# Optimization experiments

Measured on AMD Instinct MI355X. Metric: run time of the kernel, lower is better.

Reference implementation:

```python
import jax, jax.numpy as jnp
import numpy as np

D_K = 64

def setup_inputs() -> dict:
    key = jax.random.key(0)
    ks = jax.random.split(key, 8)
    B, C, H, W = 4, 256, 40, 40
    d_k, d_g, n_rel = 64, 64, 16
    s = lambda fan_in: 1.0 / np.sqrt(fan_in)
    return {
        "x":  jax.random.normal(ks[0], (B, C, H, W), jnp.float32),
        "Wq": jax.random.normal(ks[1], (C, d_k), jnp.float32) * s(C),
        "bq": jnp.zeros((d_k,), jnp.float32),
        "Wk": jax.random.normal(ks[2], (C, d_k), jnp.float32) * s(C),
        "bk": jnp.zeros((d_k,), jnp.float32),
        "Wv": jax.random.normal(ks[3], (C, C), jnp.float32) * s(C),
        "bv": jnp.zeros((C,), jnp.float32),
        "Wg1": jax.random.normal(ks[4], (4, d_g), jnp.float32) * s(4),
        "bg1": jnp.zeros((d_g,), jnp.float32),
        "Wg2": jax.random.normal(ks[5], (d_g, d_g), jnp.float32) * s(d_g),
        "bg2": jnp.zeros((d_g,), jnp.float32),
        "Wgr": jax.random.normal(ks[6], (d_g, n_rel), jnp.float32) * s(d_g),
        "bgr": jnp.zeros((n_rel,), jnp.float32),
    }

def reference(x, Wq, bq, Wk, bk, Wv, bv, Wg1, bg1, Wg2, bg2, Wgr, bgr):
    B, C, H, W = x.shape
    N = H * W
    # [B, N, C] feature tokens
    feats = jnp.transpose(x, (0, 2, 3, 1)).reshape(B, N, C)
    # pseudo-bboxes: (x, y, 1, 1) per pixel
    yy, xx = jnp.meshgrid(jnp.arange(H), jnp.arange(W), indexing="ij")
    bboxes = jnp.stack(
        [xx.astype(jnp.float32), yy.astype(jnp.float32),
         jnp.ones((H, W), jnp.float32), jnp.ones((H, W), jnp.float32)],
        axis=-1).reshape(N, 4)
    # pairwise geometric features [N, N, 4]: diff[m, n] = bboxes[n] - bboxes[m]
    diff = bboxes[None, :, :] - bboxes[:, None, :]
    geo = jnp.log(jnp.abs(diff) + 1e-8)
    # geo embedding MLP -> relation weights
    e = jax.nn.relu(geo @ Wg1 + bg1)            # [N, N, d_g]
    e = jax.nn.relu(e @ Wg2 + bg2)              # [N, N, d_g]
    w_g = jax.nn.relu(e @ Wgr + bgr)            # [N, N, n_rel]
    w_g_mean = w_g.mean(axis=2)                 # [N, N]
    # appearance attention
    q = feats @ Wq + bq                         # [B, N, d_k]
    k = feats @ Wk + bk                         # [B, N, d_k]
    w_a = jax.nn.softmax(jnp.einsum("bnd,bmd->bnm", q, k) / jnp.sqrt(jnp.float32(D_K)), axis=2)
    w_mn = w_a * w_g_mean[None]                 # [B, N, N]
    v = feats @ Wv + bv                         # [B, N, C]
    rel = jnp.einsum("bnm,bmc->bnc", w_mn, v)
    aug = feats + rel
    return jnp.transpose(aug.reshape(B, H, W, C), (0, 3, 1, 2))
```

## Files before the change

kernel.cpp:

```cpp
#include <hip/hip_runtime.h>
#include <hip/hip_bf16.h>
#include <math.h>

#define NTOK 1600
#define CDIM 256
#define DK   64

typedef __attribute__((ext_vector_type(8))) short bf16x8;
typedef __attribute__((ext_vector_type(4))) float f32x4;

__device__ inline unsigned short f2bf(float v) {
    unsigned int u = __float_as_uint(v);
    unsigned int r = (u + 0x7fffu + ((u >> 16) & 1u)) >> 16;
    return (unsigned short)r;
}

__global__ __launch_bounds__(256) void geo_table_kernel(
    const float* __restrict__ Wg1, const float* __restrict__ bg1,
    const float* __restrict__ Wg2, const float* __restrict__ bg2,
    const float* __restrict__ Wgr, const float* __restrict__ bgr,
    float* __restrict__ table)
{
    int idx = blockIdx.x * 256 + threadIdx.x;
    if (idx >= NTOK) return;
    int ady = idx / 40, adx = idx % 40;
    float g0 = logf((float)adx + 1e-8f);
    float g1 = logf((float)ady + 1e-8f);
    float gc = logf(1e-8f);

    float e1[64];
    #pragma unroll
    for (int j = 0; j < 64; ++j) {
        float t = g0 * Wg1[0*64 + j] + g1 * Wg1[1*64 + j]
                + gc * (Wg1[2*64 + j] + Wg1[3*64 + j]) + bg1[j];
        e1[j] = fmaxf(t, 0.f);
    }
    float wg[16];
    #pragma unroll
    for (int r = 0; r < 16; ++r) wg[r] = bgr[r];
    for (int j = 0; j < 64; ++j) {
        float t = bg2[j];
        #pragma unroll
        for (int i = 0; i < 64; ++i) t += e1[i] * Wg2[i*64 + j];
        t = fmaxf(t, 0.f);
        #pragma unroll
        for (int r = 0; r < 16; ++r) wg[r] += t * Wgr[j*16 + r];
    }
    float s = 0.f;
    #pragma unroll
    for (int r = 0; r < 16; ++r) s += fmaxf(wg[r], 0.f);
    table[idx] = s * (1.f / 16.f);
}

__global__ __launch_bounds__(256) void qkv_kernel(
    const float* __restrict__ x,
    const float* __restrict__ Wq, const float* __restrict__ bq,
    const float* __restrict__ Wk, const float* __restrict__ bk,
    const float* __restrict__ Wv, const float* __restrict__ bv,
    unsigned short* __restrict__ Qb, unsigned short* __restrict__ Kb,
    unsigned short* __restrict__ Vt)
{
    const int N = NTOK, C = CDIM;
    int bx = blockIdx.x;
    int jt = blockIdx.y;
    int b  = blockIdx.z;

    const float* Wm; const float* bias;
    int jb, stride;
    if (jt == 0)      { Wm = Wq; bias = bq; jb = 0;         stride = 64;  }
    else if (jt == 1) { Wm = Wk; bias = bk; jb = 0;         stride = 64;  }
    else              { Wm = Wv; bias = bv; jb = (jt-2)*64; stride = 256; }

    __shared__ __align__(16) float xs[64*68];
    __shared__ __align__(16) float wm[64*68];

    int t  = threadIdx.x;
    int tn = t & 15;
    int tj = t >> 4;
    int n0 = bx * 64;

    float acc[4][4] = {};

    for (int kc = 0; kc < 4; ++kc) {
        int k0 = kc * 64;
        #pragma unroll
        for (int p = 0; p < 4; ++p) {
            int idx4 = p*256 + t;
            int row = idx4 >> 4, col4 = (idx4 & 15) * 4;
            *(float4*)&xs[row*68 + col4] =
                *(const float4*)&x[(size_t)(b*C + k0 + row)*N + n0 + col4];
            *(float4*)&wm[row*68 + col4] =
                *(const float4*)&Wm[(size_t)(k0 + row)*stride + jb + col4];
        }
        __syncthreads();
        #pragma unroll
        for (int kk = 0; kk < 64; ++kk) {
            float4 xv = *(const float4*)(xs + kk*68 + tn*4);
            float4 wv = *(const float4*)(wm + kk*68 + tj*4);
            acc[0][0] += xv.x*wv.x; acc[0][1] += xv.x*wv.y; acc[0][2] += xv.x*wv.z; acc[0][3] += xv.x*wv.w;
            acc[1][0] += xv.y*wv.x; acc[1][1] += xv.y*wv.y; acc[1][2] += xv.y*wv.z; acc[1][3] += xv.y*wv.w;
            acc[2][0] += xv.z*wv.x; acc[2][1] += xv.z*wv.y; acc[2][2] += xv.z*wv.z; acc[2][3] += xv.z*wv.w;
            acc[3][0] += xv.w*wv.x; acc[3][1] += xv.w*wv.y; acc[3][2] += xv.w*wv.z; acc[3][3] += xv.w*wv.w;
        }
        __syncthreads();
    }

    if (jt <= 1) {
        unsigned short* outb = (jt == 0 ? Qb : Kb) + (size_t)b*N*DK;
        float scale = (jt == 0) ? 0.125f : 1.0f;
        #pragma unroll
        for (int ii = 0; ii < 4; ++ii) {
            int n = n0 + tn*4 + ii;
            __align__(8) unsigned short u[4];
            #pragma unroll
            for (int jj = 0; jj < 4; ++jj)
                u[jj] = f2bf((acc[ii][jj] + bias[tj*4 + jj]) * scale);
            *(uint2*)&outb[(size_t)n*DK + tj*4] = *(const uint2*)u;
        }
    } else {
        #pragma unroll
        for (int ii = 0; ii < 4; ++ii)
            #pragma unroll
            for (int jj = 0; jj < 4; ++jj)
                xs[(tn*4 + ii)*68 + tj*4 + jj] = acc[ii][jj] + bias[jb + tj*4 + jj];
        __syncthreads();
        int jl = t >> 2, nb = (t & 3) * 16;
        __align__(16) unsigned short u[16];
        #pragma unroll
        for (int i = 0; i < 16; ++i)
            u[i] = f2bf(xs[(nb + i)*68 + jl]);
        unsigned short* vrow = Vt + ((size_t)b*C + jb + jl)*N + n0 + nb;
        ((uint4*)vrow)[0] = ((const uint4*)u)[0];
        ((uint4*)vrow)[1] = ((const uint4*)u)[1];
    }
}

__global__ __launch_bounds__(256) void attn_mfma_kernel(
    const float* __restrict__ x, const float* __restrict__ gtab,
    const unsigned short* __restrict__ Qb, const unsigned short* __restrict__ Kb,
    const unsigned short* __restrict__ Vt, float* __restrict__ out)
{
    const int N = NTOK, C = CDIM;
    int b = blockIdx.y, n0 = blockIdx.x * 16;
    int t = threadIdx.x;
    int w = t >> 6, l = t & 63;
    int l15 = l & 15, l4 = l >> 4;

    __shared__ unsigned short Pl[2][16*72];
    __shared__ float sh_g[NTOK];
    __shared__ float shZ[4][16];
    __shared__ __align__(16) float outs[256*17];

    #pragma unroll
    for (int p = 0; p < 7; ++p) { int i = p*256 + t; if (i < NTOK) sh_g[i] = gtab[i]; }

    const unsigned short* qrow = &Qb[((size_t)b*N + n0 + l15)*DK + l4*8];
    bf16x8 qa0 = *(const bf16x8*)qrow;
    bf16x8 qa1 = *(const bf16x8*)(qrow + 32);

    f32x4 acc[4];
    #pragma unroll
    for (int i = 0; i < 4; ++i) acc[i] = (f32x4){0.f, 0.f, 0.f, 0.f};
    float z[4] = {0.f, 0.f, 0.f, 0.f};

    int yn[4], xn[4];
    #pragma unroll
    for (int r = 0; r < 4; ++r) {
        int n = n0 + l4*4 + r;
        yn[r] = n / 40; xn[r] = n - 40*yn[r];
    }
    int mcol = w*16 + l15;

    __syncthreads();

    for (int cc = 0; cc < 25; ++cc) {
        int m0 = cc * 64;
        const unsigned short* kbase = &Kb[((size_t)b*N + m0 + mcol)*DK + l4*8];
        bf16x8 kb0 = *(const bf16x8*)kbase;
        bf16x8 kb1 = *(const bf16x8*)(kbase + 32);
        f32x4 s4 = (f32x4){0.f, 0.f, 0.f, 0.f};
        s4 = __builtin_amdgcn_mfma_f32_16x16x32_bf16(qa0, kb0, s4, 0, 0, 0);
        s4 = __builtin_amdgcn_mfma_f32_16x16x32_bf16(qa1, kb1, s4, 0, 0, 0);

        int mg = m0 + mcol;
        int ym = mg / 40, xm = mg - 40*ym;
        unsigned short* prow = &Pl[cc & 1][0];
        #pragma unroll
        for (int r = 0; r < 4; ++r) {
            float e = __expf(s4[r]);
            z[r] += e;
            int ady = ym - yn[r]; ady = ady < 0 ? -ady : ady;
            int adx = xm - xn[r]; adx = adx < 0 ? -adx : adx;
            float p = e * sh_g[ady*40 + adx];
            prow[(l4*4 + r)*72 + mcol] = f2bf(p);
        }
        __syncthreads();

        const unsigned short* pb = &Pl[cc & 1][l15*72 + l4*8];
        bf16x8 pa0 = *(const bf16x8*)pb;
        bf16x8 pa1 = *(const bf16x8*)(pb + 32);
        #pragma unroll
        for (int t4 = 0; t4 < 4; ++t4) {
            int c0 = w*64 + t4*16 + l15;
            const unsigned short* vb = &Vt[((size_t)b*C + c0)*N + m0 + l4*8];
            bf16x8 v0 = *(const bf16x8*)vb;
            bf16x8 v1 = *(const bf16x8*)(vb + 32);
            acc[t4] = __builtin_amdgcn_mfma_f32_16x16x32_bf16(pa0, v0, acc[t4], 0, 0, 0);
            acc[t4] = __builtin_amdgcn_mfma_f32_16x16x32_bf16(pa1, v1, acc[t4], 0, 0, 0);
        }
    }

    #pragma unroll
    for (int r = 0; r < 4; ++r) {
        float v = z[r];
        v += __shfl_xor(v, 1); v += __shfl_xor(v, 2);
        v += __shfl_xor(v, 4); v += __shfl_xor(v, 8);
        z[r] = v;
    }
    if (l15 == 0) {
        #pragma unroll
        for (int r = 0; r < 4; ++r) shZ[w][l4*4 + r] = z[r];
    }
    __syncthreads();

    float invz[4];
    #pragma unroll
    for (int r = 0; r < 4; ++r) {
        int row = l4*4 + r;
        float s = shZ[0][row] + shZ[1][row] + shZ[2][row] + shZ[3][row];
        invz[r] = 1.f / s;
    }
    #pragma unroll
    for (int t4 = 0; t4 < 4; ++t4)
        #pragma unroll
        for (int r = 0; r < 4; ++r)
            outs[(w*64 + t4*16 + l15)*17 + l4*4 + r] = acc[t4][r] * invz[r];
    __syncthreads();

    #pragma unroll
    for (int p = 0; p < 16; ++p) {
        int c2 = p*16 + (t >> 4), r2 = t & 15;
        size_t gi = (size_t)b*C*N + (size_t)c2*N + n0 + r2;
        out[gi] = x[gi] + outs[c2*17 + r2];
    }
}

extern "C" void kernel_launch(void* const* d_in, const int* in_sizes, int n_in,
                              void* d_out, int out_size, void* d_ws, size_t ws_size,
                              hipStream_t stream)
{
    const float* x   = (const float*)d_in[0];
    const float* Wq  = (const float*)d_in[1];
    const float* bq  = (const float*)d_in[2];
    const float* Wk  = (const float*)d_in[3];
    const float* bk  = (const float*)d_in[4];
    const float* Wv  = (const float*)d_in[5];
    const float* bv  = (const float*)d_in[6];
    const float* Wg1 = (const float*)d_in[7];
    const float* bg1 = (const float*)d_in[8];
    const float* Wg2 = (const float*)d_in[9];
    const float* bg2 = (const float*)d_in[10];
    const float* Wgr = (const float*)d_in[11];
    const float* bgr = (const float*)d_in[12];

    char* ws = (char*)d_ws;
    float* table          = (float*)ws;
    unsigned short* Qb    = (unsigned short*)(ws + 8192);
    unsigned short* Kb    = (unsigned short*)(ws + 8192 + 819200);
    unsigned short* Vt    = (unsigned short*)(ws + 8192 + 2*819200);

    geo_table_kernel<<<dim3(7), dim3(256), 0, stream>>>(Wg1, bg1, Wg2, bg2, Wgr, bgr, table);
    qkv_kernel<<<dim3(25, 6, 4), dim3(256), 0, stream>>>(x, Wq, bq, Wk, bk, Wv, bv, Qb, Kb, Vt);
    attn_mfma_kernel<<<dim3(100, 4), dim3(256), 0, stream>>>(x, table, Qb, Kb, Vt, (float*)d_out);
}
```

Baseline: 209.8 us.

## Parallelize geo table, use MFMA for QKV, split attention over key chunks per wave

The geometric MLP table kernel now assigns one wave per table entry, so hidden units are computed in parallel across lanes with shared-memory staging and shuffle reductions, instead of one thread per entry with a serial 64x64 loop. The QKV projection converts x and weights to bf16 in shared memory and uses bf16 MFMA instead of scalar fp32 FMAs. The attention kernel gives each wave its own key chunks and all 256 output channels, which removes the per-chunk block barrier, and combines partial results with LDS atomics at the end. This costs more accumulator registers, atomic reduction traffic and extra bf16 rounding in the projections.

After: 204.5 us. 2.5% less time.

```diff
diff --git a/kernel.cpp b/kernel.cpp
--- a/kernel.cpp
+++ b/kernel.cpp
@@ -16,40 +16,41 @@
 }
 
 __global__ __launch_bounds__(256) void geo_table_kernel(
-    const float* __restrict__ Wg1, const float* __restrict__ bg1,
-    const float* __restrict__ Wg2, const float* __restrict__ bg2,
+    const float* __restrict__ W1, const float* __restrict__ b1,
+    const float* __restrict__ W2, const float* __restrict__ b2,
     const float* __restrict__ Wgr, const float* __restrict__ bgr,
     float* __restrict__ table)
 {
-    int idx = blockIdx.x * 256 + threadIdx.x;
-    if (idx >= NTOK) return;
+    __shared__ float e1s[4][64];
+    __shared__ float e2s[4][64];
+    int t = threadIdx.x;
+    int w = t >> 6, j = t & 63;
+    int idx = blockIdx.x * 4 + w;
     int ady = idx / 40, adx = idx % 40;
     float g0 = logf((float)adx + 1e-8f);
     float g1 = logf((float)ady + 1e-8f);
     float gc = logf(1e-8f);
 
-    float e1[64];
-    #pragma unroll
-    for (int j = 0; j < 64; ++j) {
-        float t = g0 * Wg1[0*64 + j] + g1 * Wg1[1*64 + j]
-                + gc * (Wg1[2*64 + j] + Wg1[3*64 + j]) + bg1[j];
-        e1[j] = fmaxf(t, 0.f);
-    }
-    float wg[16];
-    #pragma unroll
-    for (int r = 0; r < 16; ++r) wg[r] = bgr[r];
-    for (int j = 0; j < 64; ++j) {
-        float t = bg2[j];
-        #pragma unroll
-        for (int i = 0; i < 64; ++i) t += e1[i] * Wg2[i*64 + j];
-        t = fmaxf(t, 0.f);
-        #pragma unroll
-        for (int r = 0; r < 16; ++r) wg[r] += t * Wgr[j*16 + r];
-    }
-    float s = 0.f;
-    #pragma unroll
-    for (int r = 0; r < 16; ++r) s += fmaxf(wg[r], 0.f);
-    table[idx] = s * (1.f / 16.f);
+    float e1 = fmaxf(g0*W1[j] + g1*W1[64+j] + gc*(W1[128+j]+W1[192+j]) + b1[j], 0.f);
+    e1s[w][j] = e1;
+    __syncthreads();
+
+    float e2 = b2[j];
+    #pragma unroll 8
+    for (int i = 0; i < 64; ++i) e2 += e1s[w][i] * W2[i*64 + j];
+    e2 = fmaxf(e2, 0.f);
+    e2s[w][j] = e2;
+    __syncthreads();
+
+    int r = j & 15, q = j >> 4;
+    float v = (q == 0) ? bgr[r] : 0.f;
+    #pragma unroll
+    for (int i = 0; i < 16; ++i) v += e2s[w][q*16 + i] * Wgr[(q*16 + i)*16 + r];
+    v += __shfl_xor(v, 16); v += __shfl_xor(v, 32);
+    v = fmaxf(v, 0.f);
+    v += __shfl_xor(v, 1); v += __shfl_xor(v, 2);
+    v += __shfl_xor(v, 4); v += __shfl_xor(v, 8);
+    if (j == 0) table[idx] = v * (1.f / 16.f);
 }
 
 __global__ __launch_bounds__(256) void qkv_kernel(
@@ -60,82 +61,88 @@
     unsigned short* __restrict__ Qb, unsigned short* __restrict__ Kb,
     unsigned short* __restrict__ Vt)
 {
-    const int N = NTOK, C = CDIM;
-    int bx = blockIdx.x;
-    int jt = blockIdx.y;
-    int b  = blockIdx.z;
-
-    const float* Wm; const float* bias;
-    int jb, stride;
+    const int N = NTOK;
+    int bx = blockIdx.x, jt = blockIdx.y, b = blockIdx.z;
+    const float* Wm; const float* bias; int jb, stride;
     if (jt == 0)      { Wm = Wq; bias = bq; jb = 0;         stride = 64;  }
     else if (jt == 1) { Wm = Wk; bias = bk; jb = 0;         stride = 64;  }
     else              { Wm = Wv; bias = bv; jb = (jt-2)*64; stride = 256; }
 
-    __shared__ __align__(16) float xs[64*68];
-    __shared__ __align__(16) float wm[64*68];
-
-    int t  = threadIdx.x;
-    int tn = t & 15;
-    int tj = t >> 4;
+    __shared__ __align__(16) unsigned short As[64*72];
+    __shared__ __align__(16) unsigned short Bs[64*72];
+
+    int t = threadIdx.x;
+    int w = t >> 6, l = t & 63;
+    int l15 = l & 15, l4 = l >> 4;
     int n0 = bx * 64;
 
-    float acc[4][4] = {};
+    f32x4 acc[4];
+    #pragma unroll
+    for (int i = 0; i < 4; ++i) acc[i] = (f32x4){0.f,0.f,0.f,0.f};
 
     for (int kc = 0; kc < 4; ++kc) {
         int k0 = kc * 64;
+        __syncthreads();
         #pragma unroll
         for (int p = 0; p < 4; ++p) {
-            int idx4 = p*256 + t;
-            int row = idx4 >> 4, col4 = (idx4 & 15) * 4;
-            *(float4*)&xs[row*68 + col4] =
-                *(const float4*)&x[(size_t)(b*C + k0 + row)*N + n0 + col4];
-            *(float4*)&wm[row*68 + col4] =
-                *(const float4*)&Wm[(size_t)(k0 + row)*stride + jb + col4];
-        }
-        __syncthreads();
-        #pragma unroll
-        for (int kk = 0; kk < 64; ++kk) {
-            float4 xv = *(const float4*)(xs + kk*68 + tn*4);
-            float4 wv = *(const float4*)(wm + kk*68 + tj*4);
-            acc[0][0] += xv.x*wv.x; acc[0][1] += xv.x*wv.y; acc[0][2] += xv.x*wv.z; acc[0][3] += xv.x*wv.w;
-            acc[1][0] += xv.y*wv.x; acc[1][1] += xv.y*wv.y; acc[1][2] += xv.y*wv.z; acc[1][3] += xv.y*wv.w;
-            acc[2][0] += xv.z*wv.x; acc[2][1] += xv.z*wv.y; acc[2][2] += xv.z*wv.z; acc[2][3] += xv.z*wv.w;
-            acc[3][0] += xv.w*wv.x; acc[3][1] += xv.w*wv.y; acc[3][2] += xv.w*wv.z; acc[3][3] += xv.w*wv.w;
-        }
-        __syncthreads();
+            int k = p*16 + (t >> 4);
+            int n4 = (t & 15) * 4;
+            float4 xv = *(const float4*)&x[((size_t)(b*CDIM) + k0 + k)*N + n0 + n4];
+            As[(n4+0)*72 + k] = f2bf(xv.x); As[(n4+1)*72 + k] = f2bf(xv.y);
+            As[(n4+2)*72 + k] = f2bf(xv.z); As[(n4+3)*72 + k] = f2bf(xv.w);
+            float4 wv = *(const float4*)&Wm[(size_t)(k0 + k)*stride + jb + n4];
+            Bs[(n4+0)*72 + k] = f2bf(wv.x); Bs[(n4+1)*72 + k] = f2bf(wv.y);
+            Bs[(n4+2)*72 + k] = f2bf(wv.z); Bs[(n4+3)*72 + k] = f2bf(wv.w);
+        }
+        __syncthreads();
+        #pragma unroll
+        for (int ks = 0; ks < 2; ++ks) {
+            bf16x8 a = *(const bf16x8*)&As[(w*16 + l15)*72 + ks*32 + l4*8];
+            #pragma unroll
+            for (int jt4 = 0; jt4 < 4; ++jt4) {
+                bf16x8 bf = *(const bf16x8*)&Bs[(jt4*16 + l15)*72 + ks*32 + l4*8];
+                acc[jt4] = __builtin_amdgcn_mfma_f32_16x16x32_bf16(a, bf, acc[jt4], 0, 0, 0);
+            }
+        }
     }
 
     if (jt <= 1) {
         unsigned short* outb = (jt == 0 ? Qb : Kb) + (size_t)b*N*DK;
         float scale = (jt == 0) ? 0.125f : 1.0f;
         #pragma unroll
-        for (int ii = 0; ii < 4; ++ii) {
-            int n = n0 + tn*4 + ii;
-            __align__(8) unsigned short u[4];
-            #pragma unroll
-            for (int jj = 0; jj < 4; ++jj)
-                u[jj] = f2bf((acc[ii][jj] + bias[tj*4 + jj]) * scale);
-            *(uint2*)&outb[(size_t)n*DK + tj*4] = *(const uint2*)u;
+        for (int jt4 = 0; jt4 < 4; ++jt4) {
+            int j = jt4*16 + l15;
+            float bb = bias[j];
+            #pragma unroll
+            for (int r = 0; r < 4; ++r) {
+                int n = n0 + w*16 + l4*4 + r;
+                outb[(size_t)n*DK + j] = f2bf((acc[jt4][r] + bb) * scale);
+            }
         }
     } else {
-        #pragma unroll
-        for (int ii = 0; ii < 4; ++ii)
-            #pragma unroll
-            for (int jj = 0; jj < 4; ++jj)
-                xs[(tn*4 + ii)*68 + tj*4 + jj] = acc[ii][jj] + bias[jb + tj*4 + jj];
-        __syncthreads();
-        int jl = t >> 2, nb = (t & 3) * 16;
-        __align__(16) unsigned short u[16];
-        #pragma unroll
-        for (int i = 0; i < 16; ++i)
-            u[i] = f2bf(xs[(nb + i)*68 + jl]);
-        unsigned short* vrow = Vt + ((size_t)b*C + jb + jl)*N + n0 + nb;
-        ((uint4*)vrow)[0] = ((const uint4*)u)[0];
-        ((uint4*)vrow)[1] = ((const uint4*)u)[1];
-    }
-}
-
-__global__ __launch_bounds__(256) void attn_mfma_kernel(
+        __syncthreads();
+        unsigned short* sv = (w < 2 ? As : Bs) + (w & 1) * (64*20);
+        #pragma unroll
+        for (int jt4 = 0; jt4 < 4; ++jt4) {
+            int j = jt4*16 + l15;
+            float bb = bias[jb + j];
+            #pragma unroll
+            for (int r = 0; r < 4; ++r)
+                sv[j*20 + l4*4 + r] = f2bf(acc[jt4][r] + bb);
+        }
+        __syncthreads();
+        int c = l;
+        uint2 lo0 = *(const uint2*)&sv[c*20 + 0];
+        uint2 lo1 = *(const uint2*)&sv[c*20 + 4];
+        uint2 hi0 = *(const uint2*)&sv[c*20 + 8];
+        uint2 hi1 = *(const uint2*)&sv[c*20 + 12];
+        unsigned short* vrow = Vt + ((size_t)b*CDIM + jb + c)*N + n0 + w*16;
+        *(uint4*)(vrow)     = make_uint4(lo0.x, lo0.y, lo1.x, lo1.y);
+        *(uint4*)(vrow + 8) = make_uint4(hi0.x, hi0.y, hi1.x, hi1.y);
+    }
+}
+
+__global__ __launch_bounds__(256) void attn_kernel(
     const float* __restrict__ x, const float* __restrict__ gtab,
     const unsigned short* __restrict__ Qb, const unsigned short* __restrict__ Kb,
     const unsigned short* __restrict__ Vt, float* __restrict__ out)
@@ -146,21 +153,22 @@
     int w = t >> 6, l = t & 63;
     int l15 = l & 15, l4 = l >> 4;
 
-    __shared__ unsigned short Pl[2][16*72];
+    __shared__ __align__(16) unsigned short Pl[4][16*72];
     __shared__ float sh_g[NTOK];
-    __shared__ float shZ[4][16];
-    __shared__ __align__(16) float outs[256*17];
-
-    #pragma unroll
-    for (int p = 0; p < 7; ++p) { int i = p*256 + t; if (i < NTOK) sh_g[i] = gtab[i]; }
+    __shared__ float outs[16][260];
+    __shared__ float zs[16];
+
+    for (int p = t; p < NTOK; p += 256) sh_g[p] = gtab[p];
+    for (int p = t; p < 16*260; p += 256) ((float*)outs)[p] = 0.f;
+    if (t < 16) zs[t] = 0.f;
 
     const unsigned short* qrow = &Qb[((size_t)b*N + n0 + l15)*DK + l4*8];
     bf16x8 qa0 = *(const bf16x8*)qrow;
     bf16x8 qa1 = *(const bf16x8*)(qrow + 32);
 
-    f32x4 acc[4];
-    #pragma unroll
-    for (int i = 0; i < 4; ++i) acc[i] = (f32x4){0.f, 0.f, 0.f, 0.f};
+    f32x4 acc[16];
+    #pragma unroll
+    for (int i = 0; i < 16; ++i) acc[i] = (f32x4){0.f,0.f,0.f,0.f};
     float z[4] = {0.f, 0.f, 0.f, 0.f};
 
     int yn[4], xn[4];
@@ -169,44 +177,41 @@
         int n = n0 + l4*4 + r;
         yn[r] = n / 40; xn[r] = n - 40*yn[r];
     }
-    int mcol = w*16 + l15;
-
-    __syncthreads();
-
-    for (int cc = 0; cc < 25; ++cc) {
+
+    __syncthreads();
+
+    unsigned short* Pw = &Pl[w][0];
+
+    for (int cc = w; cc < 25; cc += 4) {
         int m0 = cc * 64;
-        const unsigned short* kbase = &Kb[((size_t)b*N + m0 + mcol)*DK + l4*8];
-        bf16x8 kb0 = *(const bf16x8*)kbase;
-        bf16x8 kb1 = *(const bf16x8*)(kbase + 32);
-        f32x4 s4 = (f32x4){0.f, 0.f, 0.f, 0.f};
-        s4 = __builtin_amdgcn_mfma_f32_16x16x32_bf16(qa0, kb0, s4, 0, 0, 0);
-        s4 = __builtin_amdgcn_mfma_f32_16x16x32_bf16(qa1, kb1, s4, 0, 0, 0);
-
-        int mg = m0 + mcol;
-        int ym = mg / 40, xm = mg - 40*ym;
-        unsigned short* prow = &Pl[cc & 1][0];
-        #pragma unroll
-        for (int r = 0; r < 4; ++r) {
-            float e = __expf(s4[r]);
-            z[r] += e;
-            int ady = ym - yn[r]; ady = ady < 0 ? -ady : ady;
-            int adx = xm - xn[r]; adx = adx < 0 ? -adx : adx;
-            float p = e * sh_g[ady*40 + adx];
-            prow[(l4*4 + r)*72 + mcol] = f2bf(p);
-        }
-        __syncthreads();
-
-        const unsigned short* pb = &Pl[cc & 1][l15*72 + l4*8];
-        bf16x8 pa0 = *(const bf16x8*)pb;
-        bf16x8 pa1 = *(const bf16x8*)(pb + 32);
-        #pragma unroll
-        for (int t4 = 0; t4 < 4; ++t4) {
-            int c0 = w*64 + t4*16 + l15;
-            const unsigned short* vb = &Vt[((size_t)b*C + c0)*N + m0 + l4*8];
+        #pragma unroll
+        for (int tt = 0; tt < 4; ++tt) {
+            int mg = m0 + tt*16 + l15;
+            const unsigned short* kbase = &Kb[((size_t)b*N + mg)*DK + l4*8];
+            bf16x8 kb0 = *(const bf16x8*)kbase;
+            bf16x8 kb1 = *(const bf16x8*)(kbase + 32);
+            f32x4 s4 = (f32x4){0.f,0.f,0.f,0.f};
+            s4 = __builtin_amdgcn_mfma_f32_16x16x32_bf16(qa0, kb0, s4, 0, 0, 0);
+            s4 = __builtin_amdgcn_mfma_f32_16x16x32_bf16(qa1, kb1, s4, 0, 0, 0);
+            int ym = mg / 40, xm = mg - 40*ym;
+            #pragma unroll
+            for (int r = 0; r < 4; ++r) {
+                float e = __expf(s4[r]);
+                z[r] += e;
+                int ady = ym - yn[r]; ady = ady < 0 ? -ady : ady;
+                int adx = xm - xn[r]; adx = adx < 0 ? -adx : adx;
+                Pw[(l4*4 + r)*72 + tt*16 + l15] = f2bf(e * sh_g[ady*40 + adx]);
+            }
+        }
+        bf16x8 pa0 = *(const bf16x8*)&Pw[l15*72 + l4*8];
+        bf16x8 pa1 = *(const bf16x8*)&Pw[l15*72 + 32 + l4*8];
+        #pragma unroll
+        for (int ct = 0; ct < 16; ++ct) {
+            const unsigned short* vb = &Vt[((size_t)b*C + ct*16 + l15)*N + m0 + l4*8];
             bf16x8 v0 = *(const bf16x8*)vb;
             bf16x8 v1 = *(const bf16x8*)(vb + 32);
-            acc[t4] = __builtin_amdgcn_mfma_f32_16x16x32_bf16(pa0, v0, acc[t4], 0, 0, 0);
-            acc[t4] = __builtin_amdgcn_mfma_f32_16x16x32_bf16(pa1, v1, acc[t4], 0, 0, 0);
+            acc[ct] = __builtin_amdgcn_mfma_f32_16x16x32_bf16(pa0, v0, acc[ct], 0, 0, 0);
+            acc[ct] = __builtin_amdgcn_mfma_f32_16x16x32_bf16(pa1, v1, acc[ct], 0, 0, 0);
         }
     }
 
@@ -215,33 +220,22 @@
         float v = z[r];
         v += __shfl_xor(v, 1); v += __shfl_xor(v, 2);
         v += __shfl_xor(v, 4); v += __shfl_xor(v, 8);
-        z[r] = v;
-    }
-    if (l15 == 0) {
-        #pragma unroll
-        for (int r = 0; r < 4; ++r) shZ[w][l4*4 + r] = z[r];
-    }
-    __syncthreads();
-
-    float invz[4];
-    #pragma unroll
-    for (int r = 0; r < 4; ++r) {
-        int row = l4*4 + r;
-        float s = shZ[0][row] + shZ[1][row] + shZ[2][row] + shZ[3][row];
-        invz[r] = 1.f / s;
-    }
-    #pragma unroll
-    for (int t4 = 0; t4 < 4; ++t4)
+        if (l15 == 0) atomicAdd(&zs[l4*4 + r], v);
+    }
+    #pragma unroll
+    for (int ct = 0; ct < 16; ++ct)
         #pragma unroll
         for (int r = 0; r < 4; ++r)
-            outs[(w*64 + t4*16 + l15)*17 + l4*4 + r] = acc[t4][r] * invz[r];
-    __syncthreads();
-
+            atomicAdd(&outs[l4*4 + r][ct*16 + l15], acc[ct][r]);
+    __syncthreads();
+
+    int r2 = t & 15;
+    float invz = 1.f / zs[r2];
     #pragma unroll
     for (int p = 0; p < 16; ++p) {
-        int c2 = p*16 + (t >> 4), r2 = t & 15;
-        size_t gi = (size_t)b*C*N + (size_t)c2*N + n0 + r2;
-        out[gi] = x[gi] + outs[c2*17 + r2];
+        int c2 = p*16 + (t >> 4);
+        size_t gi = ((size_t)b*C + c2)*N + n0 + r2;
+        out[gi] = x[gi] + outs[r2][c2] * invz;
     }
 }
 
@@ -264,12 +258,12 @@
     const float* bgr = (const float*)d_in[12];
 
     char* ws = (char*)d_ws;
-    float* table          = (float*)ws;
-    unsigned short* Qb    = (unsigned short*)(ws + 8192);
-    unsigned short* Kb    = (unsigned short*)(ws + 8192 + 819200);
-    unsigned short* Vt    = (unsigned short*)(ws + 8192 + 2*819200);
-
-    geo_table_kernel<<<dim3(7), dim3(256), 0, stream>>>(Wg1, bg1, Wg2, bg2, Wgr, bgr, table);
+    float* table       = (float*)ws;
+    unsigned short* Qb = (unsigned short*)(ws + 8192);
+    unsigned short* Kb = (unsigned short*)(ws + 8192 + 819200);
+    unsigned short* Vt = (unsigned short*)(ws + 8192 + 2*819200);
+
+    geo_table_kernel<<<dim3(400), dim3(256), 0, stream>>>(Wg1, bg1, Wg2, bg2, Wgr, bgr, table);
     qkv_kernel<<<dim3(25, 6, 4), dim3(256), 0, stream>>>(x, Wq, bq, Wk, bk, Wv, bv, Qb, Kb, Vt);
-    attn_mfma_kernel<<<dim3(100, 4), dim3(256), 0, stream>>>(x, table, Qb, Kb, Vt, (float*)d_out);
-}
+    attn_kernel<<<dim3(100, 4), dim3(256), 0, stream>>>(x, table, Qb, Kb, Vt, (float*)d_out);
+}
```
